# Performance work log

Hardware: AMD Instinct MI355X
Metric: run time of the kernel (lower is better)

## Reference

```python
import jax, jax.numpy as jnp
import numpy as np

N = 50000
E = 625000
IN_NODE = 128
IN_EDGE = 64
H = 128
OUT = 112
L = 3


def setup_inputs() -> dict:
    key = jax.random.key(0)
    ks = jax.random.split(key, 16)
    s = lambda fan_in: 1.0 / np.sqrt(fan_in)
    inp = {
        "x": jax.random.normal(ks[0], (N, IN_NODE), jnp.float32),
        "edge_attr": jax.random.normal(ks[1], (E, IN_EDGE), jnp.float32),
        "edge_index": jax.random.randint(ks[2], (2, E), 0, N, jnp.int32),
        # encoders
        "node_W": jax.random.uniform(ks[3], (IN_NODE, H), jnp.float32, -s(IN_NODE), s(IN_NODE)),
        "node_b": jnp.zeros((H,), jnp.float32),
        "edge_W": jax.random.uniform(ks[4], (IN_EDGE, H), jnp.float32, -s(IN_EDGE), s(IN_EDGE)),
        "edge_b": jnp.zeros((H,), jnp.float32),
        # per-layer GINConv MLP params, stacked over layers
        "W1": jax.random.uniform(ks[5], (L, H, 2 * H), jnp.float32, -s(H), s(H)),
        "b1": jnp.zeros((L, 2 * H), jnp.float32),
        "W2": jax.random.uniform(ks[6], (L, 2 * H, H), jnp.float32, -s(2 * H), s(2 * H)),
        "b2": jnp.zeros((L, H), jnp.float32),
        "eps": jnp.zeros((L,), jnp.float32),
        # output head
        "lin_W": jax.random.uniform(ks[7], (H, OUT), jnp.float32, -s(H), s(H)),
        "lin_b": jnp.zeros((OUT,), jnp.float32),
    }
    return inp


def reference(x, edge_attr, edge_index, node_W, node_b, edge_W, edge_b,
              W1, b1, W2, b2, eps, lin_W, lin_b):
    src = edge_index[0]  # x_j gather indices (source nodes)
    dst = edge_index[1]  # scatter targets
    n = x.shape[0]

    x = x @ node_W + node_b                 # [N, H]
    ea = edge_attr @ edge_W + edge_b        # [E, H]

    # in-degree for mean aggregation (clamped at 1, zero-degree -> 0 agg)
    deg = jax.ops.segment_sum(jnp.ones((src.shape[0],), x.dtype), dst, num_segments=n)
    inv_deg = 1.0 / jnp.maximum(deg, 1.0)   # [N]

    for l in range(L):
        msg = x[src] + ea                                    # [E, H]
        agg = jax.ops.segment_sum(msg, dst, num_segments=n)  # [N, H]
        agg = agg * inv_deg[:, None]                         # mean
        h = (1.0 + eps[l]) * x + agg
        h = jax.nn.relu(h @ W1[l] + b1[l]) @ W2[l] + b2[l]   # GIN MLP
        x = jax.nn.relu(h)                                   # dropout is identity in eval

    return x @ lin_W + lin_b                 # [N, OUT]
```

## Files before the change

kernel.cpp:

```cpp
#include <hip/hip_runtime.h>


typedef unsigned short u16;
typedef unsigned int   u32;

using short8 = __attribute__((ext_vector_type(8))) short;
using f32x4  = __attribute__((ext_vector_type(4))) float;

__device__ __forceinline__ float b2f(u16 u) {
  union { u32 i; float f; } v; v.i = ((u32)u) << 16; return v.f;
}
__device__ __forceinline__ u16 f2b(float f) {
  union { float f; u32 i; } v; v.f = f;
  u32 i = v.i;
  return (u16)((i + 0x7FFFu + ((i >> 16) & 1u)) >> 16);
}

__global__ void sniff_kernel(const u16* __restrict__ xu, int* __restrict__ flag) {
  __shared__ int cnt;
  if (threadIdx.x == 0) cnt = 0;
  __syncthreads();
  int c = 0;
  for (int i = threadIdx.x; i < 1024; i += 256) {
    int e = (xu[i] >> 7) & 0xFF;
    if (e >= 100 && e <= 140) c++;
  }
  atomicAdd(&cnt, c);
  __syncthreads();
  if (threadIdx.x == 0) *flag = (cnt >= 820) ? 1 : 0;
}

__global__ void cvt_bf16_kernel(const void* __restrict__ src, u16* __restrict__ dst,
                                int n, const int* __restrict__ flag) {
  int i = blockIdx.x * 256 + threadIdx.x;
  if (i >= n) return;
  if (*flag) dst[i] = ((const u16*)src)[i];
  else       dst[i] = f2b(((const float*)src)[i]);
}

__global__ void transpose_cvt_kernel(const void* __restrict__ src, u16* __restrict__ dst,
                                     int K, int N, int total, const int* __restrict__ flag) {
  int i = blockIdx.x * 256 + threadIdx.x;
  if (i >= total) return;
  int kn = K * N;
  int l = i / kn, r = i - l * kn;
  int k = r / N, n = r - k * N;
  u16 v = (*flag) ? ((const u16*)src)[i] : f2b(((const float*)src)[i]);
  dst[(size_t)l * kn + n * K + k] = v;
}

struct BiasJobs { const void* src[6]; float* dst[6]; int len[6]; };
__global__ void cvt_bias_kernel(BiasJobs j, const int* __restrict__ flag) {
  int b = blockIdx.x;
  int isbf = *flag;
  for (int i = threadIdx.x; i < j.len[b]; i += 256) {
    j.dst[b][i] = isbf ? b2f(((const u16*)j.src[b])[i]) : ((const float*)j.src[b])[i];
  }
}

__global__ void deg_kernel(const int* __restrict__ dst, int* __restrict__ deg, int e) {
  int i = blockIdx.x * 256 + threadIdx.x;
  if (i < e) atomicAdd(&deg[dst[i]], 1);
}

__global__ void scanA_kernel(const int* __restrict__ deg, int* __restrict__ rowptr,
                             float* __restrict__ invdeg, int* __restrict__ btot, int n) {
  __shared__ int wsum[4];
  int tid = threadIdx.x, lane = tid & 63, wid = tid >> 6;
  int i = blockIdx.x * 256 + tid;
  int v = (i < n) ? deg[i] : 0;
  int incl = v;
  #pragma unroll
  for (int off = 1; off < 64; off <<= 1) {
    int t = __shfl_up(incl, off, 64);
    if (lane >= off) incl += t;
  }
  if (lane == 63) wsum[wid] = incl;
  __syncthreads();
  int woff = 0;
  for (int w = 0; w < wid; ++w) woff += wsum[w];
  if (i < n) {
    rowptr[i] = woff + incl - v;
    invdeg[i] = 1.0f / fmaxf((float)v, 1.0f);
  }
  if (tid == 255) btot[blockIdx.x] = woff + incl;
}

__global__ void scanB_kernel(int* __restrict__ btot, int nb) {
  __shared__ int wsum[4];
  int tid = threadIdx.x, lane = tid & 63, wid = tid >> 6;
  int v = (tid < nb) ? btot[tid] : 0;
  int incl = v;
  #pragma unroll
  for (int off = 1; off < 64; off <<= 1) {
    int t = __shfl_up(incl, off, 64);
    if (lane >= off) incl += t;
  }
  if (lane == 63) wsum[wid] = incl;
  __syncthreads();
  int woff = 0;
  for (int w = 0; w < wid; ++w) woff += wsum[w];
  if (tid < nb) btot[tid] = woff + incl - v;
}

__global__ void scanC_kernel(int* __restrict__ rowptr, const int* __restrict__ btot,
                             int n, int e) {
  int i = blockIdx.x * 256 + threadIdx.x;
  if (i < n) rowptr[i] += btot[blockIdx.x];
  if (i == 0) rowptr[n] = e;
}

__global__ void fill_kernel(const int* __restrict__ src, const int* __restrict__ dst,
                            const int* __restrict__ rowptr, int* __restrict__ fillc,
                            int* __restrict__ csr_src, int e) {
  int i = blockIdx.x * 256 + threadIdx.x;
  if (i < e) {
    int d = dst[i];
    int p = rowptr[d] + atomicAdd(&fillc[d], 1);
    csr_src[p] = src[i];
  }
}

__global__ __launch_bounds__(256) void scatter_kernel(
    const void* __restrict__ ea, const int* __restrict__ dst,
    float* __restrict__ sattr, int e, const int* __restrict__ flag) {
  int eg = blockIdx.x * 4 + (threadIdx.x >> 6);
  int lane = threadIdx.x & 63;
  if (eg >= e) return;
  int d = dst[eg];
  float v;
  if (*flag) v = b2f(((const u16*)ea)[(size_t)eg * 64 + lane]);
  else       v = ((const float*)ea)[(size_t)eg * 64 + lane];
  atomicAdd(&sattr[(size_t)d * 64 + lane], v);
}

template <int K, int N, int ACT, int MODE>
__global__ __launch_bounds__(256) void gemm_kernel(
    const void* __restrict__ Av, const u16* __restrict__ WT,
    const float* __restrict__ bias, void* __restrict__ Cv, int M,
    const int* __restrict__ flag, const float* __restrict__ rowscale,
    const int* __restrict__ degp) {
  constexpr int KC = 64;
  constexpr int KCP = KC + 8;
  constexpr int NF = N / 16;
  constexpr int NV = N * KC / 8;
  static_assert(K % KC == 0 && N % 16 == 0, "dims");
  __shared__ u16 WS[N * KCP];

  int tid = threadIdx.x, lane = tid & 63, wid = tid >> 6;
  int row0 = blockIdx.x * 64 + wid * 16;
  int arow = row0 + (lane & 15);
  if (arow >= M) arow = M - 1;

  f32x4 acc[NF];
  #pragma unroll
  for (int i = 0; i < NF; ++i) acc[i] = (f32x4){0.f, 0.f, 0.f, 0.f};

  for (int kc0 = 0; kc0 < K; kc0 += KC) {
    #pragma unroll
    for (int v = tid; v < NV; v += 256) {
      int n = v >> 3, k8 = (v & 7) << 3;
      *reinterpret_cast<short8*>(&WS[n * KCP + k8]) =
          *reinterpret_cast<const short8*>(&WT[(size_t)n * K + kc0 + k8]);
    }
    __syncthreads();
    #pragma unroll
    for (int ks = 0; ks < KC; ks += 32) {
      short8 a;
      if (MODE == 2) {
        const float* Af = (const float*)Av + (size_t)arow * K + kc0 + ((lane >> 4) * 8) + ks;
        f32x4 a0 = *reinterpret_cast<const f32x4*>(Af);
        f32x4 a1 = *reinterpret_cast<const f32x4*>(Af + 4);
        #pragma unroll
        for (int q = 0; q < 4; ++q) { a[q] = (short)f2b(a0[q]); a[q + 4] = (short)f2b(a1[q]); }
      } else {
        const u16* Ab = (const u16*)Av + (size_t)arow * K + kc0 + ((lane >> 4) * 8) + ks;
        a = *reinterpret_cast<const short8*>(Ab);
      }
      #pragma unroll
      for (int nf = 0; nf < NF; ++nf) {
        const u16* bp = &WS[(nf * 16 + (lane & 15)) * KCP + ks + ((lane >> 4) * 8)];
        short8 b = *reinterpret_cast<const short8*>(bp);
        acc[nf] = __builtin_amdgcn_mfma_f32_16x16x32_bf16(a, b, acc[nf], 0, 0, 0);
      }
    }
    __syncthreads();
  }

  int isbf = 1;
  if (MODE == 1) isbf = *flag;
  int crow0 = row0 + ((lane >> 4) * 4);
  #pragma unroll
  for (int nf = 0; nf < NF; ++nf) {
    int col = nf * 16 + (lane & 15);
    float bv = bias[col];
    #pragma unroll
    for (int r = 0; r < 4; ++r) {
      int crow = crow0 + r;
      if (crow < M) {
        size_t idx = (size_t)crow * N + col;
        if (MODE == 2) {
          float v = acc[nf][r] * rowscale[crow] + (degp[crow] > 0 ? bv : 0.f);
          ((float*)Cv)[idx] = v;
        } else {
          float v = acc[nf][r] + bv;
          if (ACT) v = fmaxf(v, 0.f);
          if (MODE == 1 && !isbf) ((float*)Cv)[idx] = v;
          else                    ((u16*)Cv)[idx]   = f2b(v);
        }
      }
    }
  }
}

__global__ __launch_bounds__(256) void agg_kernel(
    const u16* __restrict__ xcur, const int* __restrict__ rowptr,
    const int* __restrict__ csr_src, const float* __restrict__ invdeg,
    const float* __restrict__ seab, const float* __restrict__ epsf, int l,
    u16* __restrict__ h0, int nnodes) {
  int tid = threadIdx.x, lane = tid & 63, wid = tid >> 6;
  int node = blockIdx.x * 4 + wid;
  if (node >= nnodes) return;
  const u32* xc = (const u32*)xcur;
  int r0 = rowptr[node], r1 = rowptr[node + 1];
  float p0 = 0.f, p1 = 0.f, q0 = 0.f, q1 = 0.f, s0 = 0.f, s1 = 0.f, t0 = 0.f, t1 = 0.f;
  int j = r0;
  for (; j + 4 <= r1; j += 4) {
    int sa = csr_src[j], sb = csr_src[j + 1], sc = csr_src[j + 2], sd = csr_src[j + 3];
    u32 va = xc[(size_t)sa * 64 + lane];
    u32 vb = xc[(size_t)sb * 64 + lane];
    u32 vc = xc[(size_t)sc * 64 + lane];
    u32 vd = xc[(size_t)sd * 64 + lane];
    p0 += b2f((u16)(va & 0xffff)); p1 += b2f((u16)(va >> 16));
    q0 += b2f((u16)(vb & 0xffff)); q1 += b2f((u16)(vb >> 16));
    s0 += b2f((u16)(vc & 0xffff)); s1 += b2f((u16)(vc >> 16));
    t0 += b2f((u16)(vd & 0xffff)); t1 += b2f((u16)(vd >> 16));
  }
  for (; j < r1; ++j) {
    int s = csr_src[j];
    u32 v = xc[(size_t)s * 64 + lane];
    p0 += b2f((u16)(v & 0xffff)); p1 += b2f((u16)(v >> 16));
  }
  float a0 = (p0 + q0) + (s0 + t0);
  float a1 = (p1 + q1) + (s1 + t1);
  float epl = 1.0f + epsf[l];
  float iv = invdeg[node];
  u32 xv = xc[(size_t)node * 64 + lane];
  float h0v = epl * b2f((u16)(xv & 0xffff)) + a0 * iv + seab[(size_t)node * 128 + lane * 2];
  float h1v = epl * b2f((u16)(xv >> 16))    + a1 * iv + seab[(size_t)node * 128 + lane * 2 + 1];
  u32 packed = (u32)f2b(h0v) | ((u32)f2b(h1v) << 16);
  *reinterpret_cast<u32*>(&h0[(size_t)node * 128 + lane * 2]) = packed;
}

extern "C" void kernel_launch(void* const* d_in, const int* in_sizes, int n_in,
                              void* d_out, int out_size, void* d_ws, size_t ws_size,
                              hipStream_t stream) {
  const void* x_in  = d_in[0];
  const void* eattr = d_in[1];
  const int*  eidx  = (const int*)d_in[2];
  const void* nodeW = d_in[3];
  const void* nodeb = d_in[4];
  const void* edgeW = d_in[5];
  const void* edgeb = d_in[6];
  const void* W1    = d_in[7];
  const void* b1    = d_in[8];
  const void* W2    = d_in[9];
  const void* b2    = d_in[10];
  const void* eps   = d_in[11];
  const void* linW  = d_in[12];
  const void* linb  = d_in[13];

  int nn = in_sizes[0] / 128;
  int ne = in_sizes[2] / 2;

  char* ws = (char*)d_ws;
  size_t off = 0;
  auto alloc = [&](size_t b) { size_t r = off; off += (b + 255) & ~(size_t)255; return r; };
  int*    flag    = (int*)(ws + alloc(4));
  int*    deg     = (int*)(ws + alloc((size_t)nn * 4));
  int*    fillc   = (int*)(ws + alloc((size_t)nn * 4));
  int*    rowptr  = (int*)(ws + alloc((size_t)(nn + 1) * 4));
  float*  invdeg  = (float*)(ws + alloc((size_t)nn * 4));
  int*    btot    = (int*)(ws + alloc(256 * 4));
  int*    csr_src = (int*)(ws + alloc((size_t)ne * 4));
  float*  sattr   = (float*)(ws + alloc((size_t)nn * 64 * 4));
  float*  seab    = (float*)(ws + alloc((size_t)nn * 128 * 4));
  u16*    xb      = (u16*)(ws + alloc((size_t)nn * 128 * 2));
  u16*    xcur    = (u16*)(ws + alloc((size_t)nn * 128 * 2));
  u16*    h0      = (u16*)(ws + alloc((size_t)nn * 128 * 2));
  u16*    tbuf    = (u16*)(ws + alloc((size_t)nn * 256 * 2));
  u16*    nodeWT  = (u16*)(ws + alloc(128 * 128 * 2));
  u16*    edgeWT  = (u16*)(ws + alloc(64 * 128 * 2));
  u16*    W1T     = (u16*)(ws + alloc((size_t)3 * 128 * 256 * 2));
  u16*    W2T     = (u16*)(ws + alloc((size_t)3 * 256 * 128 * 2));
  u16*    linWT   = (u16*)(ws + alloc(128 * 112 * 2));
  float*  nodebf  = (float*)(ws + alloc(128 * 4));
  float*  edgebf  = (float*)(ws + alloc(128 * 4));
  float*  b1f     = (float*)(ws + alloc(3 * 256 * 4));
  float*  b2f_    = (float*)(ws + alloc(3 * 128 * 4));
  float*  epsf    = (float*)(ws + alloc(3 * 4));
  float*  linbf   = (float*)(ws + alloc(112 * 4));

  hipMemsetAsync(deg, 0, (size_t)nn * 4, stream);
  hipMemsetAsync(fillc, 0, (size_t)nn * 4, stream);
  hipMemsetAsync(sattr, 0, (size_t)nn * 64 * 4, stream);

  sniff_kernel<<<1, 256, 0, stream>>>((const u16*)x_in, flag);

  cvt_bf16_kernel<<<(nn * 128 + 255) / 256, 256, 0, stream>>>(x_in, xb, nn * 128, flag);
  auto tcv = [&](const void* s, u16* d, int K, int N, int L) {
    int tot = L * K * N;
    transpose_cvt_kernel<<<(tot + 255) / 256, 256, 0, stream>>>(s, d, K, N, tot, flag);
  };
  tcv(nodeW, nodeWT, 128, 128, 1);
  tcv(edgeW, edgeWT, 64, 128, 1);
  tcv(W1, W1T, 128, 256, 3);
  tcv(W2, W2T, 256, 128, 3);
  tcv(linW, linWT, 128, 112, 1);

  BiasJobs bj;
  bj.src[0] = nodeb; bj.dst[0] = nodebf; bj.len[0] = 128;
  bj.src[1] = edgeb; bj.dst[1] = edgebf; bj.len[1] = 128;
  bj.src[2] = b1;    bj.dst[2] = b1f;    bj.len[2] = 3 * 256;
  bj.src[3] = b2;    bj.dst[3] = b2f_;   bj.len[3] = 3 * 128;
  bj.src[4] = eps;   bj.dst[4] = epsf;   bj.len[4] = 3;
  bj.src[5] = linb;  bj.dst[5] = linbf;  bj.len[5] = 112;
  cvt_bias_kernel<<<6, 256, 0, stream>>>(bj, flag);

  int eb = (ne + 255) / 256;
  int nb = (nn + 255) / 256;
  deg_kernel<<<eb, 256, 0, stream>>>(eidx + ne, deg, ne);
  scanA_kernel<<<nb, 256, 0, stream>>>(deg, rowptr, invdeg, btot, nn);
  scanB_kernel<<<1, 256, 0, stream>>>(btot, nb);
  scanC_kernel<<<nb, 256, 0, stream>>>(rowptr, btot, nn, ne);
  fill_kernel<<<eb, 256, 0, stream>>>(eidx, eidx + ne, rowptr, fillc, csr_src, ne);

  scatter_kernel<<<(ne + 3) / 4, 256, 0, stream>>>(eattr, eidx + ne, sattr, ne, flag);

  int gb = (nn + 63) / 64;
  gemm_kernel<128, 128, 0, 0><<<gb, 256, 0, stream>>>(xb, nodeWT, nodebf, xcur, nn, flag, nullptr, nullptr);
  gemm_kernel<64, 128, 0, 2><<<gb, 256, 0, stream>>>(sattr, edgeWT, edgebf, seab, nn, flag, invdeg, deg);

  for (int l = 0; l < 3; ++l) {
    agg_kernel<<<(nn + 3) / 4, 256, 0, stream>>>(xcur, rowptr, csr_src, invdeg, seab, epsf, l, h0, nn);
    gemm_kernel<128, 256, 1, 0><<<gb, 256, 0, stream>>>(h0, W1T + (size_t)l * 128 * 256,
                                                        b1f + l * 256, tbuf, nn, flag, nullptr, nullptr);
    gemm_kernel<256, 128, 1, 0><<<gb, 256, 0, stream>>>(tbuf, W2T + (size_t)l * 256 * 128,
                                                        b2f_ + l * 128, xcur, nn, flag, nullptr, nullptr);
  }
  gemm_kernel<128, 112, 0, 1><<<gb, 256, 0, stream>>>(xcur, linWT, linbf, d_out, nn, flag, nullptr, nullptr);
}
```

Baseline: 743.7 us.

## Replace atomic edge-attr scatter with CSR gather; double GEMM rows per wave

The per-edge atomicAdd scatter of edge attributes is replaced by a per-node gather over a new CSR edge-id array, which also removes the sattr memset. Each wave splits into two half-wave groups that cover alternate edges and combine with a shuffle. The GEMM kernel now processes 32 rows per wave (128 per block), reusing each LDS B fragment for two MFMAs and halving the number of weight staging loads per row. The aggregation loop is unrolled to 8 gathers in flight with a single accumulator pair. The cost is an extra csr_eid buffer and its writes, plus higher register use in the GEMM.

After: 719.0 us. 3.3% less time.

```diff
diff --git a/kernel.cpp b/kernel.cpp
--- a/kernel.cpp
+++ b/kernel.cpp
@@ -6,6 +6,7 @@
 
 using short8 = __attribute__((ext_vector_type(8))) short;
 using f32x4  = __attribute__((ext_vector_type(4))) float;
+using f32x2  = __attribute__((ext_vector_type(2))) float;
 
 __device__ __forceinline__ float b2f(u16 u) {
   union { u32 i; float f; } v; v.i = ((u32)u) << 16; return v.f;
@@ -112,26 +113,68 @@
 
 __global__ void fill_kernel(const int* __restrict__ src, const int* __restrict__ dst,
                             const int* __restrict__ rowptr, int* __restrict__ fillc,
-                            int* __restrict__ csr_src, int e) {
+                            int* __restrict__ csr_src, int* __restrict__ csr_eid, int e) {
   int i = blockIdx.x * 256 + threadIdx.x;
   if (i < e) {
     int d = dst[i];
     int p = rowptr[d] + atomicAdd(&fillc[d], 1);
     csr_src[p] = src[i];
-  }
-}
-
-__global__ __launch_bounds__(256) void scatter_kernel(
-    const void* __restrict__ ea, const int* __restrict__ dst,
-    float* __restrict__ sattr, int e, const int* __restrict__ flag) {
-  int eg = blockIdx.x * 4 + (threadIdx.x >> 6);
-  int lane = threadIdx.x & 63;
-  if (eg >= e) return;
-  int d = dst[eg];
-  float v;
-  if (*flag) v = b2f(((const u16*)ea)[(size_t)eg * 64 + lane]);
-  else       v = ((const float*)ea)[(size_t)eg * 64 + lane];
-  atomicAdd(&sattr[(size_t)d * 64 + lane], v);
+    csr_eid[p] = i;
+  }
+}
+
+__global__ __launch_bounds__(256) void sattr_gather_kernel(
+    const void* __restrict__ ea, const int* __restrict__ rowptr,
+    const int* __restrict__ csr_eid, float* __restrict__ sattr,
+    int nnodes, const int* __restrict__ flag) {
+  int tid = threadIdx.x, lane = tid & 63, wid = tid >> 6;
+  int node = blockIdx.x * 4 + wid;
+  if (node >= nnodes) return;
+  int hl = lane >> 5, l32 = lane & 31;
+  int r0 = rowptr[node], r1 = rowptr[node + 1];
+  int isbf = *flag;
+  float s0 = 0.f, s1 = 0.f;
+  if (isbf) {
+    const u32* ea32 = (const u32*)ea;
+    int j = r0 + hl;
+    for (; j + 6 < r1; j += 8) {
+      int e0 = csr_eid[j], e1 = csr_eid[j + 2], e2 = csr_eid[j + 4], e3 = csr_eid[j + 6];
+      u32 v0 = ea32[(size_t)e0 * 32 + l32];
+      u32 v1 = ea32[(size_t)e1 * 32 + l32];
+      u32 v2 = ea32[(size_t)e2 * 32 + l32];
+      u32 v3 = ea32[(size_t)e3 * 32 + l32];
+      s0 += b2f((u16)(v0 & 0xffff)) + b2f((u16)(v1 & 0xffff)) +
+            b2f((u16)(v2 & 0xffff)) + b2f((u16)(v3 & 0xffff));
+      s1 += b2f((u16)(v0 >> 16)) + b2f((u16)(v1 >> 16)) +
+            b2f((u16)(v2 >> 16)) + b2f((u16)(v3 >> 16));
+    }
+    for (; j < r1; j += 2) {
+      u32 v = ea32[(size_t)csr_eid[j] * 32 + l32];
+      s0 += b2f((u16)(v & 0xffff));
+      s1 += b2f((u16)(v >> 16));
+    }
+  } else {
+    const f32x2* eaf = (const f32x2*)ea;
+    int j = r0 + hl;
+    for (; j + 6 < r1; j += 8) {
+      f32x2 v0 = eaf[(size_t)csr_eid[j] * 32 + l32];
+      f32x2 v1 = eaf[(size_t)csr_eid[j + 2] * 32 + l32];
+      f32x2 v2 = eaf[(size_t)csr_eid[j + 4] * 32 + l32];
+      f32x2 v3 = eaf[(size_t)csr_eid[j + 6] * 32 + l32];
+      s0 += v0.x + v1.x + v2.x + v3.x;
+      s1 += v0.y + v1.y + v2.y + v3.y;
+    }
+    for (; j < r1; j += 2) {
+      f32x2 v = eaf[(size_t)csr_eid[j] * 32 + l32];
+      s0 += v.x; s1 += v.y;
+    }
+  }
+  s0 += __shfl_xor(s0, 32, 64);
+  s1 += __shfl_xor(s1, 32, 64);
+  if (hl == 0) {
+    f32x2 o; o.x = s0; o.y = s1;
+    *reinterpret_cast<f32x2*>(&sattr[(size_t)node * 64 + l32 * 2]) = o;
+  }
 }
 
 template <int K, int N, int ACT, int MODE>
@@ -148,13 +191,16 @@
   __shared__ u16 WS[N * KCP];
 
   int tid = threadIdx.x, lane = tid & 63, wid = tid >> 6;
-  int row0 = blockIdx.x * 64 + wid * 16;
-  int arow = row0 + (lane & 15);
-  if (arow >= M) arow = M - 1;
-
-  f32x4 acc[NF];
+  int lane16 = lane & 15, lh = lane >> 4;
+  int row0 = blockIdx.x * 128 + wid * 32;
+  int arow0 = row0 + lane16;       if (arow0 >= M) arow0 = M - 1;
+  int arow1 = row0 + 16 + lane16;  if (arow1 >= M) arow1 = M - 1;
+
+  f32x4 acc[2][NF];
   #pragma unroll
-  for (int i = 0; i < NF; ++i) acc[i] = (f32x4){0.f, 0.f, 0.f, 0.f};
+  for (int rb = 0; rb < 2; ++rb)
+    #pragma unroll
+    for (int i = 0; i < NF; ++i) acc[rb][i] = (f32x4){0.f, 0.f, 0.f, 0.f};
 
   for (int kc0 = 0; kc0 < K; kc0 += KC) {
     #pragma unroll
@@ -166,22 +212,28 @@
     __syncthreads();
     #pragma unroll
     for (int ks = 0; ks < KC; ks += 32) {
-      short8 a;
+      short8 a0, a1;
       if (MODE == 2) {
-        const float* Af = (const float*)Av + (size_t)arow * K + kc0 + ((lane >> 4) * 8) + ks;
-        f32x4 a0 = *reinterpret_cast<const f32x4*>(Af);
-        f32x4 a1 = *reinterpret_cast<const f32x4*>(Af + 4);
+        const float* Af0 = (const float*)Av + (size_t)arow0 * K + kc0 + ks + lh * 8;
+        const float* Af1 = (const float*)Av + (size_t)arow1 * K + kc0 + ks + lh * 8;
+        f32x4 p0 = *reinterpret_cast<const f32x4*>(Af0);
+        f32x4 p1 = *reinterpret_cast<const f32x4*>(Af0 + 4);
+        f32x4 q0 = *reinterpret_cast<const f32x4*>(Af1);
+        f32x4 q1 = *reinterpret_cast<const f32x4*>(Af1 + 4);
         #pragma unroll
-        for (int q = 0; q < 4; ++q) { a[q] = (short)f2b(a0[q]); a[q + 4] = (short)f2b(a1[q]); }
+        for (int q = 0; q < 4; ++q) {
+          a0[q] = (short)f2b(p0[q]); a0[q + 4] = (short)f2b(p1[q]);
+          a1[q] = (short)f2b(q0[q]); a1[q + 4] = (short)f2b(q1[q]);
+        }
       } else {
-        const u16* Ab = (const u16*)Av + (size_t)arow * K + kc0 + ((lane >> 4) * 8) + ks;
-        a = *reinterpret_cast<const short8*>(Ab);
+        a0 = *reinterpret_cast<const short8*>((const u16*)Av + (size_t)arow0 * K + kc0 + ks + lh * 8);
+        a1 = *reinterpret_cast<const short8*>((const u16*)Av + (size_t)arow1 * K + kc0 + ks + lh * 8);
       }
       #pragma unroll
       for (int nf = 0; nf < NF; ++nf) {
-        const u16* bp = &WS[(nf * 16 + (lane & 15)) * KCP + ks + ((lane >> 4) * 8)];
-        short8 b = *reinterpret_cast<const short8*>(bp);
-        acc[nf] = __builtin_amdgcn_mfma_f32_16x16x32_bf16(a, b, acc[nf], 0, 0, 0);
+        short8 b = *reinterpret_cast<const short8*>(&WS[(nf * 16 + lane16) * KCP + ks + lh * 8]);
+        acc[0][nf] = __builtin_amdgcn_mfma_f32_16x16x32_bf16(a0, b, acc[0][nf], 0, 0, 0);
+        acc[1][nf] = __builtin_amdgcn_mfma_f32_16x16x32_bf16(a1, b, acc[1][nf], 0, 0, 0);
       }
     }
     __syncthreads();
@@ -189,24 +241,26 @@
 
   int isbf = 1;
   if (MODE == 1) isbf = *flag;
-  int crow0 = row0 + ((lane >> 4) * 4);
   #pragma unroll
-  for (int nf = 0; nf < NF; ++nf) {
-    int col = nf * 16 + (lane & 15);
-    float bv = bias[col];
+  for (int rb = 0; rb < 2; ++rb) {
+    int crow0 = row0 + rb * 16 + lh * 4;
     #pragma unroll
-    for (int r = 0; r < 4; ++r) {
-      int crow = crow0 + r;
-      if (crow < M) {
-        size_t idx = (size_t)crow * N + col;
-        if (MODE == 2) {
-          float v = acc[nf][r] * rowscale[crow] + (degp[crow] > 0 ? bv : 0.f);
-          ((float*)Cv)[idx] = v;
-        } else {
-          float v = acc[nf][r] + bv;
-          if (ACT) v = fmaxf(v, 0.f);
-          if (MODE == 1 && !isbf) ((float*)Cv)[idx] = v;
-          else                    ((u16*)Cv)[idx]   = f2b(v);
+    for (int nf = 0; nf < NF; ++nf) {
+      int col = nf * 16 + lane16;
+      float bv = bias[col];
+      #pragma unroll
+      for (int r = 0; r < 4; ++r) {
+        int crow = crow0 + r;
+        if (crow < M) {
+          size_t idx = (size_t)crow * N + col;
+          if (MODE == 2) {
+            ((float*)Cv)[idx] = acc[rb][nf][r] * rowscale[crow] + (degp[crow] > 0 ? bv : 0.f);
+          } else {
+            float v = acc[rb][nf][r] + bv;
+            if (ACT) v = fmaxf(v, 0.f);
+            if (MODE == 1 && !isbf) ((float*)Cv)[idx] = v;
+            else                    ((u16*)Cv)[idx]   = f2b(v);
+          }
         }
       }
     }
@@ -223,26 +277,33 @@
   if (node >= nnodes) return;
   const u32* xc = (const u32*)xcur;
   int r0 = rowptr[node], r1 = rowptr[node + 1];
-  float p0 = 0.f, p1 = 0.f, q0 = 0.f, q1 = 0.f, s0 = 0.f, s1 = 0.f, t0 = 0.f, t1 = 0.f;
+  float a0 = 0.f, a1 = 0.f;
   int j = r0;
-  for (; j + 4 <= r1; j += 4) {
-    int sa = csr_src[j], sb = csr_src[j + 1], sc = csr_src[j + 2], sd = csr_src[j + 3];
-    u32 va = xc[(size_t)sa * 64 + lane];
-    u32 vb = xc[(size_t)sb * 64 + lane];
-    u32 vc = xc[(size_t)sc * 64 + lane];
-    u32 vd = xc[(size_t)sd * 64 + lane];
-    p0 += b2f((u16)(va & 0xffff)); p1 += b2f((u16)(va >> 16));
-    q0 += b2f((u16)(vb & 0xffff)); q1 += b2f((u16)(vb >> 16));
-    s0 += b2f((u16)(vc & 0xffff)); s1 += b2f((u16)(vc >> 16));
-    t0 += b2f((u16)(vd & 0xffff)); t1 += b2f((u16)(vd >> 16));
+  for (; j + 8 <= r1; j += 8) {
+    int s0 = csr_src[j],     s1 = csr_src[j + 1], s2 = csr_src[j + 2], s3 = csr_src[j + 3];
+    int s4 = csr_src[j + 4], s5 = csr_src[j + 5], s6 = csr_src[j + 6], s7 = csr_src[j + 7];
+    u32 v0 = xc[(size_t)s0 * 64 + lane];
+    u32 v1 = xc[(size_t)s1 * 64 + lane];
+    u32 v2 = xc[(size_t)s2 * 64 + lane];
+    u32 v3 = xc[(size_t)s3 * 64 + lane];
+    u32 v4 = xc[(size_t)s4 * 64 + lane];
+    u32 v5 = xc[(size_t)s5 * 64 + lane];
+    u32 v6 = xc[(size_t)s6 * 64 + lane];
+    u32 v7 = xc[(size_t)s7 * 64 + lane];
+    a0 += ((b2f((u16)(v0 & 0xffff)) + b2f((u16)(v1 & 0xffff))) +
+           (b2f((u16)(v2 & 0xffff)) + b2f((u16)(v3 & 0xffff)))) +
+          ((b2f((u16)(v4 & 0xffff)) + b2f((u16)(v5 & 0xffff))) +
+           (b2f((u16)(v6 & 0xffff)) + b2f((u16)(v7 & 0xffff))));
+    a1 += ((b2f((u16)(v0 >> 16)) + b2f((u16)(v1 >> 16))) +
+           (b2f((u16)(v2 >> 16)) + b2f((u16)(v3 >> 16)))) +
+          ((b2f((u16)(v4 >> 16)) + b2f((u16)(v5 >> 16))) +
+           (b2f((u16)(v6 >> 16)) + b2f((u16)(v7 >> 16))));
   }
   for (; j < r1; ++j) {
-    int s = csr_src[j];
-    u32 v = xc[(size_t)s * 64 + lane];
-    p0 += b2f((u16)(v & 0xffff)); p1 += b2f((u16)(v >> 16));
-  }
-  float a0 = (p0 + q0) + (s0 + t0);
-  float a1 = (p1 + q1) + (s1 + t1);
+    u32 v = xc[(size_t)csr_src[j] * 64 + lane];
+    a0 += b2f((u16)(v & 0xffff));
+    a1 += b2f((u16)(v >> 16));
+  }
   float epl = 1.0f + epsf[l];
   float iv = invdeg[node];
   u32 xv = xc[(size_t)node * 64 + lane];
@@ -283,6 +344,7 @@
   float*  invdeg  = (float*)(ws + alloc((size_t)nn * 4));
   int*    btot    = (int*)(ws + alloc(256 * 4));
   int*    csr_src = (int*)(ws + alloc((size_t)ne * 4));
+  int*    csr_eid = (int*)(ws + alloc((size_t)ne * 4));
   float*  sattr   = (float*)(ws + alloc((size_t)nn * 64 * 4));
   float*  seab    = (float*)(ws + alloc((size_t)nn * 128 * 4));
   u16*    xb      = (u16*)(ws + alloc((size_t)nn * 128 * 2));
@@ -303,7 +365,6 @@
 
   hipMemsetAsync(deg, 0, (size_t)nn * 4, stream);
   hipMemsetAsync(fillc, 0, (size_t)nn * 4, stream);
-  hipMemsetAsync(sattr, 0, (size_t)nn * 64 * 4, stream);
 
   sniff_kernel<<<1, 256, 0, stream>>>((const u16*)x_in, flag);
 
@@ -333,11 +394,11 @@
   scanA_kernel<<<nb, 256, 0, stream>>>(deg, rowptr, invdeg, btot, nn);
   scanB_kernel<<<1, 256, 0, stream>>>(btot, nb);
   scanC_kernel<<<nb, 256, 0, stream>>>(rowptr, btot, nn, ne);
-  fill_kernel<<<eb, 256, 0, stream>>>(eidx, eidx + ne, rowptr, fillc, csr_src, ne);
-
-  scatter_kernel<<<(ne + 3) / 4, 256, 0, stream>>>(eattr, eidx + ne, sattr, ne, flag);
-
-  int gb = (nn + 63) / 64;
+  fill_kernel<<<eb, 256, 0, stream>>>(eidx, eidx + ne, rowptr, fillc, csr_src, csr_eid, ne);
+
+  sattr_gather_kernel<<<(nn + 3) / 4, 256, 0, stream>>>(eattr, rowptr, csr_eid, sattr, nn, flag);
+
+  int gb = (nn + 127) / 128;
   gemm_kernel<128, 128, 0, 0><<<gb, 256, 0, stream>>>(xb, nodeWT, nodebf, xcur, nn, flag, nullptr, nullptr);
   gemm_kernel<64, 128, 0, 2><<<gb, 256, 0, stream>>>(sattr, edgeWT, edgebf, seab, nn, flag, invdeg, deg);
 
```
